# Performance work log

Hardware: AMD Instinct MI355X
Metric: run time of the kernel (lower is better)

## Reference

```python
import jax, jax.numpy as jnp
import numpy as np

BASELINE = 0.24  # vertical stereo baseline used in the original forward


def setup_inputs() -> dict:
    key = jax.random.key(0)
    k1, k2, k3 = jax.random.split(key, 3)
    bs, C, H, W = 1, 16, 256, 512
    ndisp = 32
    x = jax.random.normal(k1, (bs, C, H, W), dtype=jnp.float32)
    y = jax.random.normal(k2, (bs, C, H, W), dtype=jnp.float32)
    depth = jax.random.uniform(k3, (bs, ndisp, H, W), dtype=jnp.float32,
                               minval=0.5, maxval=8.0)
    return {"x": x, "y": y, "depth_range_samples": depth, "ndisp": ndisp}


def _theta_rows(height):
    # spherical latitude per pixel row (equirectangular, pixel-centered),
    # theta in (-pi/2, pi/2) -- S360.grid.create_spherical_grid channel 1
    v = (jnp.arange(height, dtype=jnp.float32) + 0.5) * (np.pi / height) - np.pi / 2
    return v[None, None, :, None]  # [1,1,H,1]


def _dtheta_vertical(theta, depth, baseline, height):
    # S360.derivatives.dtheta_vertical: angular shift of a scene point at
    # (theta, depth) seen from a camera displaced vertically by `baseline`,
    # converted from radians to pixel rows.
    dth = jnp.arctan((depth * jnp.sin(theta) + baseline) / (depth * jnp.cos(theta))) - theta
    return dth * (height / np.pi)


def _grid_sample_bilinear_zeros(img, grid):
    # Faithful F.grid_sample(mode='bilinear', padding_mode='zeros',
    # align_corners=False). img [B,C,H,W]; grid [B,Hg,Wg,2] in [-1,1].
    B, C, H, W = img.shape
    ix = ((grid[..., 0] + 1.0) * W - 1.0) * 0.5  # unnormalize (align_corners=False)
    iy = ((grid[..., 1] + 1.0) * H - 1.0) * 0.5
    x0 = jnp.floor(ix)
    y0 = jnp.floor(iy)
    wx1 = ix - x0
    wy1 = iy - y0
    img_flat = img.reshape(B, C, H * W)

    def corner(xi, yi, w):
        valid = (xi >= 0) & (xi <= W - 1) & (yi >= 0) & (yi <= H - 1)
        xc = jnp.clip(xi, 0, W - 1).astype(jnp.int32)
        yc = jnp.clip(yi, 0, H - 1).astype(jnp.int32)
        flat = yc * W + xc                                   # [B,Hg,Wg]
        v = jax.vmap(lambda im, f: im[:, f])(img_flat, flat)  # [B,C,Hg,Wg]
        return v * (w * valid.astype(img.dtype))[:, None]

    return (corner(x0,     y0,     (1 - wx1) * (1 - wy1))
          + corner(x0 + 1, y0,     wx1       * (1 - wy1))
          + corner(x0,     y0 + 1, (1 - wx1) * wy1)
          + corner(x0 + 1, y0 + 1, wx1       * wy1))


def reference(x, y, depth_range_samples, ndisp):
    bs, C, H, W = x.shape
    theta = _theta_rows(H)                                   # [1,1,H,1]
    d_v = _dtheta_vertical(theta, depth_range_samples, BASELINE, H)  # [bs,nd,H,W]
    v = jnp.arange(H, dtype=x.dtype)[None, None, :, None]
    u = jnp.arange(W, dtype=x.dtype)[None, None, None, :]
    # torch zeroes NaN/Inf entries of (uvgrid + disp); x-coords (disp_x=0) stay u
    y_px = jnp.where(jnp.isfinite(d_v), v + d_v, 0.0)        # [bs,nd,H,W]
    coords_x = jnp.broadcast_to(u / ((W - 1.0) / 2.0) - 1.0, y_px.shape)
    coords_y = y_px / ((H - 1.0) / 2.0) - 1.0
    grid = jnp.stack([coords_x, coords_y], axis=-1)          # [bs,nd,H,W,2]
    warped = _grid_sample_bilinear_zeros(y, grid.reshape(bs, ndisp * H, W, 2))
    warped = warped.reshape(bs, C, ndisp, H, W)
    ref = jnp.broadcast_to(x[:, :, None], (bs, C, ndisp, H, W))
    return jnp.concatenate([ref, warped], axis=1)            # [bs,2C,nd,H,W]
```

## Files before the change

kernel.cpp:

```cpp
#include <hip/hip_runtime.h>
#include <math.h>

#define CCH 16
#define HH 256
#define WW 512
#define ND 32
#define HWSZ (HH * WW)
#define BASELINE 0.24f

__global__ __launch_bounds__(256) void cost_volume_kernel(
    const float* __restrict__ x,
    const float* __restrict__ y,
    const float* __restrict__ depth,
    float* __restrict__ out)
{
    int tid = blockIdx.x * blockDim.x + threadIdx.x;
    if (tid >= ND * HWSZ) return;

    int w = tid & (WW - 1);
    int h = (tid >> 9) & (HH - 1);
    int d = tid >> 17;
    int p = h * WW + w;

    float dep = depth[d * HWSZ + p];

    float theta = ((float)h + 0.5f) * (float)(M_PI / HH) - (float)(M_PI / 2.0);
    float st, ct;
    sincosf(theta, &st, &ct);

    float dth = atanf((dep * st + BASELINE) / (dep * ct)) - theta;
    float d_v = dth * (float)(HH / M_PI);
    float y_px = isfinite(d_v) ? ((float)h + d_v) : 0.0f;

    float cx = (float)w / ((WW - 1.0f) * 0.5f) - 1.0f;
    float cy = y_px   / ((HH - 1.0f) * 0.5f) - 1.0f;
    float ix = ((cx + 1.0f) * (float)WW - 1.0f) * 0.5f;
    float iy = ((cy + 1.0f) * (float)HH - 1.0f) * 0.5f;

    float x0f = floorf(ix);
    float y0f = floorf(iy);
    float wx1 = ix - x0f;
    float wy1 = iy - y0f;
    float wx0 = 1.0f - wx1;
    float wy0 = 1.0f - wy1;

    int x0 = (int)x0f;
    int y0 = (int)y0f;
    int x1 = x0 + 1;
    int y1 = y0 + 1;

    float vx0 = (x0 >= 0 && x0 <= WW - 1) ? 1.0f : 0.0f;
    float vx1 = (x1 >= 0 && x1 <= WW - 1) ? 1.0f : 0.0f;
    float vy0 = (y0 >= 0 && y0 <= HH - 1) ? 1.0f : 0.0f;
    float vy1 = (y1 >= 0 && y1 <= HH - 1) ? 1.0f : 0.0f;

    int x0c = min(max(x0, 0), WW - 1);
    int x1c = min(max(x1, 0), WW - 1);
    int y0c = min(max(y0, 0), HH - 1);
    int y1c = min(max(y1, 0), HH - 1);

    float w00 = wx0 * wy0 * vx0 * vy0;
    float w10 = wx1 * wy0 * vx1 * vy0;
    float w01 = wx0 * wy1 * vx0 * vy1;
    float w11 = wx1 * wy1 * vx1 * vy1;

    int f00 = y0c * WW + x0c;
    int f10 = y0c * WW + x1c;
    int f01 = y1c * WW + x0c;
    int f11 = y1c * WW + x1c;

    int dp = d * HWSZ + p;

    #pragma unroll
    for (int c = 0; c < CCH; ++c) {
        int cb = c * HWSZ;
        float v00 = y[cb + f00];
        float v10 = y[cb + f10];
        float v01 = y[cb + f01];
        float v11 = y[cb + f11];
        float val = v00 * w00 + v10 * w10 + v01 * w01 + v11 * w11;

        out[(size_t)(c * ND) * HWSZ + dp] = x[cb + p];
        out[(size_t)((CCH + c) * ND) * HWSZ + dp] = val;
    }
}

extern "C" void kernel_launch(void* const* d_in, const int* in_sizes, int n_in,
                              void* d_out, int out_size, void* d_ws, size_t ws_size,
                              hipStream_t stream) {
    const float* x = (const float*)d_in[0];
    const float* y = (const float*)d_in[1];
    const float* depth = (const float*)d_in[2];
    float* out = (float*)d_out;

    int total = ND * HWSZ;
    int block = 256;
    int grid = (total + block - 1) / block;
    cost_volume_kernel<<<grid, block, 0, stream>>>(x, y, depth, out);
}
```

Baseline: 729.6 us.

## Transpose y to channel-last layout for vectorized bilinear gathers

Adds a pre-pass that converts y from channel-planar to per-pixel channel-contiguous layout in workspace. The sampling kernel can then fetch all 16 channels of each bilinear corner with four float4 loads instead of 16 scattered scalar loads. The launch is also remapped to a 3D grid so each block covers a 64-wide row segment for 4 depths, which aims to improve cache reuse of x and y. The cost is an extra kernel launch and dependence on a sufficiently large workspace.

```diff
diff --git a/kernel.cpp b/kernel.cpp
--- a/kernel.cpp
+++ b/kernel.cpp
@@ -8,18 +8,29 @@
 #define HWSZ (HH * WW)
 #define BASELINE 0.24f
 
+__global__ __launch_bounds__(256) void transpose_y_kernel(
+    const float* __restrict__ y, float* __restrict__ yt)
+{
+    int p = blockIdx.x * blockDim.x + threadIdx.x;
+    if (p >= HWSZ) return;
+    float v[CCH];
+    #pragma unroll
+    for (int c = 0; c < CCH; ++c) v[c] = y[c * HWSZ + p];
+    float4* dst = (float4*)(yt + (size_t)p * CCH);
+    #pragma unroll
+    for (int j = 0; j < 4; ++j)
+        dst[j] = make_float4(v[4 * j], v[4 * j + 1], v[4 * j + 2], v[4 * j + 3]);
+}
+
 __global__ __launch_bounds__(256) void cost_volume_kernel(
     const float* __restrict__ x,
-    const float* __restrict__ y,
+    const float4* __restrict__ yt4,
     const float* __restrict__ depth,
     float* __restrict__ out)
 {
-    int tid = blockIdx.x * blockDim.x + threadIdx.x;
-    if (tid >= ND * HWSZ) return;
-
-    int w = tid & (WW - 1);
-    int h = (tid >> 9) & (HH - 1);
-    int d = tid >> 17;
+    int w = blockIdx.x * 64 + (threadIdx.x & 63);
+    int h = blockIdx.y;
+    int d = blockIdx.z * 4 + (threadIdx.x >> 6);
     int p = h * WW + w;
 
     float dep = depth[d * HWSZ + p];
@@ -64,24 +75,43 @@
     float w01 = wx0 * wy1 * vx0 * vy1;
     float w11 = wx1 * wy1 * vx1 * vy1;
 
-    int f00 = y0c * WW + x0c;
-    int f10 = y0c * WW + x1c;
-    int f01 = y1c * WW + x0c;
-    int f11 = y1c * WW + x1c;
+    int b00 = (y0c * WW + x0c) * 4;
+    int b10 = (y0c * WW + x1c) * 4;
+    int b01 = (y1c * WW + x0c) * 4;
+    int b11 = (y1c * WW + x1c) * 4;
 
-    int dp = d * HWSZ + p;
+    float4 acc[4];
+    #pragma unroll
+    for (int j = 0; j < 4; ++j) {
+        float4 a = yt4[b00 + j];
+        acc[j] = make_float4(a.x * w00, a.y * w00, a.z * w00, a.w * w00);
+    }
+    #pragma unroll
+    for (int j = 0; j < 4; ++j) {
+        float4 a = yt4[b10 + j];
+        acc[j].x += a.x * w10; acc[j].y += a.y * w10;
+        acc[j].z += a.z * w10; acc[j].w += a.w * w10;
+    }
+    #pragma unroll
+    for (int j = 0; j < 4; ++j) {
+        float4 a = yt4[b01 + j];
+        acc[j].x += a.x * w01; acc[j].y += a.y * w01;
+        acc[j].z += a.z * w01; acc[j].w += a.w * w01;
+    }
+    #pragma unroll
+    for (int j = 0; j < 4; ++j) {
+        float4 a = yt4[b11 + j];
+        acc[j].x += a.x * w11; acc[j].y += a.y * w11;
+        acc[j].z += a.z * w11; acc[j].w += a.w * w11;
+    }
+
+    const float* accf = (const float*)acc;
+    size_t dp = (size_t)d * HWSZ + p;
 
     #pragma unroll
     for (int c = 0; c < CCH; ++c) {
-        int cb = c * HWSZ;
-        float v00 = y[cb + f00];
-        float v10 = y[cb + f10];
-        float v01 = y[cb + f01];
-        float v11 = y[cb + f11];
-        float val = v00 * w00 + v10 * w10 + v01 * w01 + v11 * w11;
-
-        out[(size_t)(c * ND) * HWSZ + dp] = x[cb + p];
-        out[(size_t)((CCH + c) * ND) * HWSZ + dp] = val;
+        out[(size_t)c * (ND * HWSZ) + dp] = x[c * HWSZ + p];
+        out[(size_t)(CCH + c) * (ND * HWSZ) + dp] = accf[c];
     }
 }
 
@@ -92,9 +122,10 @@
     const float* y = (const float*)d_in[1];
     const float* depth = (const float*)d_in[2];
     float* out = (float*)d_out;
+    float* yt = (float*)d_ws;
 
-    int total = ND * HWSZ;
-    int block = 256;
-    int grid = (total + block - 1) / block;
-    cost_volume_kernel<<<grid, block, 0, stream>>>(x, y, depth, out);
+    transpose_y_kernel<<<(HWSZ + 255) / 256, 256, 0, stream>>>(y, yt);
+
+    dim3 grid(WW / 64, HH, ND / 4);
+    cost_volume_kernel<<<grid, 256, 0, stream>>>(x, (const float4*)yt, depth, out);
 }
```

New measurement: 663.4 us. 1.1x faster.
